# Optimization experiments

Measured on AMD Instinct MI355X. Metric: run time of the kernel, lower is better.

The kernel has to match this reference:

```python
import jax, jax.numpy as jnp
import numpy as np
from jax import lax

# Fixed dims from MSSMamba defaults
B_, L_, DM = 2, 8192, 256
NH, HP, NS = 4, 64, 8          # nheads, headdim, d_state
DIN = NH * HP                  # d_inner = 256
DPROJ = 2 * DIN + 2 * NS + NH  # 532


def setup_inputs() -> dict:
    key = jax.random.key(0)
    ks = jax.random.split(key, 16)
    f = lambda k, s, sc=1.0: jax.random.normal(k, s, jnp.float32) * sc
    inp = {
        'x_H': f(ks[0], (B_, L_, DM)),
        'x_V': f(ks[1], (B_, L_, DM)),
        'W_in_H': f(ks[2], (DM, 2 * DPROJ), 0.05),
        'W_in_V': f(ks[3], (DM, 2 * DPROJ), 0.05),
        'W_out_HF': f(ks[4], (DIN, DM), 0.05),
        'W_out_HB': f(ks[5], (DIN, DM), 0.05),
        'W_out_VF': f(ks[6], (DIN, DM), 0.05),
        'W_out_VB': f(ks[7], (DIN, DM), 0.05),
        'W_out': f(ks[8], (4 * DM, DM), 0.05),
    }
    for i, nm in enumerate(['HF', 'HB', 'VF', 'VB']):
        kd = jax.random.fold_in(ks[9], i)
        ka = jax.random.fold_in(ks[10], i)
        inp['dt_bias_' + nm] = f(kd, (NH,), 0.1)
        inp['A_log_' + nm] = jnp.log(jax.random.uniform(ka, (NH,), jnp.float32, 1.0, 16.0))
        inp['D_' + nm] = jnp.ones((NH,), jnp.float32)
    # per-batch permutation mapping vertical position -> horizontal position
    inp['v2h'] = jax.vmap(lambda k: jax.random.permutation(k, L_))(
        jax.random.split(ks[11], B_)).astype(jnp.int32)
    return inp


def _scan_dir(zxbcdt, dt_bias, A_log, D):
    # zxbcdt: [b, l, DPROJ] -> Mamba2-style selective scan, ngroups=1
    z = zxbcdt[..., :DIN].reshape(B_, L_, NH, HP)
    xBC = jax.nn.silu(zxbcdt[..., DIN:DIN + DIN + 2 * NS])
    x = xBC[..., :DIN].reshape(B_, L_, NH, HP)
    Bm = xBC[..., DIN:DIN + NS]      # [b, l, n]
    Cm = xBC[..., DIN + NS:]         # [b, l, n]
    dt = jax.nn.softplus(zxbcdt[..., -NH:] + dt_bias)  # [b, l, h]
    A = -jnp.exp(A_log)              # [h]
    dA = jnp.exp(dt * A)             # [b, l, h]
    dBx = jnp.einsum('blh,bln,blhp->blhpn', dt, Bm, x)  # [b,l,h,p,n]

    def step(state, inp):
        dA_t, dBx_t, C_t = inp
        state = dA_t[..., None, None] * state + dBx_t   # [b,h,p,n]
        y_t = jnp.einsum('bhpn,bn->bhp', state, C_t)
        return state, y_t

    init = jnp.zeros((B_, NH, HP, NS), dt.dtype)
    _, ys = lax.scan(step, init, (jnp.moveaxis(dA, 1, 0),
                                  jnp.moveaxis(dBx, 1, 0),
                                  jnp.moveaxis(Cm, 1, 0)))
    y = jnp.moveaxis(ys, 0, 1) + D[None, None, :, None] * x  # skip D*x
    y = y * jax.nn.silu(z)                                   # gate
    return y.reshape(B_, L_, DIN)


def reference(x_H, x_V, W_in_H, W_in_V,
              dt_bias_HF, dt_bias_HB, dt_bias_VF, dt_bias_VB,
              A_log_HF, A_log_HB, A_log_VF, A_log_VB,
              D_HF, D_HB, D_VF, D_VB,
              W_out_HF, W_out_HB, W_out_VF, W_out_VB,
              W_out, v2h):
    zx_HF, zx_HB = jnp.split(x_H @ W_in_H, 2, axis=-1)
    zx_VF, zx_VB = jnp.split(x_V @ W_in_V, 2, axis=-1)
    # note: source applies out_proj_HB to the HF branch (kept faithful)
    y_HF = _scan_dir(zx_HF, dt_bias_HF, A_log_HF, D_HF) @ W_out_HB
    y_HB = _scan_dir(zx_HB[:, ::-1], dt_bias_HB, A_log_HB, D_HB)[:, ::-1] @ W_out_HF
    y_VF = _scan_dir(zx_VF, dt_bias_VF, A_log_VF, D_VF) @ W_out_VB
    y_VB = _scan_dir(zx_VB[:, ::-1], dt_bias_VB, A_log_VB, D_VB)[:, ::-1] @ W_out_VF
    # remap vertical-ordered outputs to horizontal ordering (scatter by v2h)
    bidx = jnp.arange(B_)[:, None]
    y_VF = jnp.zeros_like(y_VF).at[bidx, v2h].set(y_VF)
    y_VB = jnp.zeros_like(y_VB).at[bidx, v2h].set(y_VB)
    cat = jnp.concatenate([y_HF, y_HB, y_VF, y_VB], axis=-1)  # [b, l, 4*d_model]
    return jax.nn.silu(cat) @ W_out
```

## Files before the change

### kernel.cpp

```cpp
#include <hip/hip_runtime.h>
#include <hip/hip_bf16.h>

#define B_N 2
#define L_N 8192
#define ROWS 16384
#define CHUNK 32
#define NCHUNK 256
#define GRP 16
#define NGRP 16
#define NPAD 1152

typedef __bf16 bf16x8 __attribute__((ext_vector_type(8)));
typedef float f32x4 __attribute__((ext_vector_type(4)));

__device__ __forceinline__ float siluf(float v) {
  return v * __builtin_amdgcn_rcpf(1.f + __expf(-v));
}
__device__ __forceinline__ float softplusf_(float v) {
  return fmaxf(v, 0.f) + log1pf(__expf(-fabsf(v)));
}
__device__ __forceinline__ unsigned short f2bf(float v) {
  union { __bf16 b; unsigned short u; } x;
  x.b = (__bf16)v;
  return x.u;
}
__device__ __forceinline__ float bf2f(unsigned short u) {
  union { unsigned u; float f; } x; x.u = ((unsigned)u) << 16;
  return x.f;
}

__device__ __forceinline__ void gload_lds16(const unsigned short* g, unsigned short* l) {
  __builtin_amdgcn_global_load_lds(
      (const __attribute__((address_space(1))) unsigned int*)g,
      (__attribute__((address_space(3))) unsigned int*)l, 16, 0, 0);
}

struct P4 { const float* p[4]; };
struct ScanConsts {
  const float* dt_bias[4];
  const float* A_log[4];
  const float* D[4];
};

__global__ __launch_bounds__(256) void k_prep(
    const float* __restrict__ xH, const float* __restrict__ xV,
    const float* __restrict__ WH, const float* __restrict__ WV,
    P4 ws, const float* __restrict__ W_out, const int* __restrict__ v2h, ScanConsts sc,
    unsigned short* __restrict__ xbf, float* __restrict__ dtv_arr, float* __restrict__ dA_arr,
    unsigned short* __restrict__ Wt_in, unsigned short* __restrict__ Wt_dirs,
    unsigned short* __restrict__ Wt_fin, int* __restrict__ inv) {
  __shared__ float xs[32][257];
  __shared__ float Wsm[8][260];
  int bid = blockIdx.x;
  int tid = threadIdx.x;
  if (bid < 1024) {
    const int mat = bid >> 9;
    const float* x = mat ? xV : xH;
    const float* W = mat ? WV : WH;
    const int r0 = (bid & 511) * 32;
    for (int i = tid; i < 2048; i += 256) {
      int c = i >> 8, k = i & 255;
      int sl = c >> 2, h = c & 3;
      Wsm[c][k] = W[(long)k * 1064 + sl * 532 + 528 + h];
    }
    for (int i = tid; i < 32 * 64; i += 256) {
      int rl = i >> 6, kq = (i & 63) * 4;
      float4 v = *(const float4*)(x + (long)(r0 + rl) * 256 + kq);
      xs[rl][kq + 0] = v.x; xs[rl][kq + 1] = v.y; xs[rl][kq + 2] = v.z; xs[rl][kq + 3] = v.w;
    }
    __syncthreads();
    for (int i = tid; i < 32 * 64; i += 256) {
      int rl = i >> 6, kq = (i & 63) * 4;
      ushort4 o;
      o.x = f2bf(xs[rl][kq + 0]);
      o.y = f2bf(xs[rl][kq + 1]);
      o.z = f2bf(xs[rl][kq + 2]);
      o.w = f2bf(xs[rl][kq + 3]);
      *(ushort4*)(xbf + (size_t)mat * ROWS * 256 + (long)(r0 + rl) * 256 + kq) = o;
    }
    const int rl = tid >> 3, c = tid & 7;
    float s = 0.f;
    #pragma unroll 8
    for (int k = 0; k < 256; ++k) s = fmaf(xs[rl][k], Wsm[c][k], s);
    const int sl = c >> 2, h = c & 3;
    const int dir = mat * 2 + sl;
    float dtv = softplusf_(s + sc.dt_bias[dir][h]);
    float dAv = __expf(dtv * (-__expf(sc.A_log[dir][h])));
    long o = ((long)dir * 4 + h) * ROWS + (r0 + rl);
    dtv_arr[o] = dtv;
    dA_arr[o] = dAv;
  } else if (bid < 3328) {
    int i = (bid - 1024) * 256 + tid;
    int z = i / (NPAD * 256);
    int rem = i - z * (NPAD * 256);
    int n = rem >> 8, k = rem & 255;
    const float* W = z ? WV : WH;
    int sl = n >= 544;
    int cc = n - (sl ? 544 : 0);
    float v = (cc < 532) ? W[(long)k * 1064 + sl * 532 + cc] : 0.f;
    Wt_in[i] = f2bf(v);
  } else if (bid < 4352) {
    int i = (bid - 3328) * 256 + tid;
    int d = i >> 16;
    int rem = i & 65535;
    int n = rem >> 8, k = rem & 255;
    Wt_dirs[i] = f2bf(ws.p[d][(long)k * 256 + n]);
  } else if (bid < 5376) {
    int i = (bid - 4352) * 256 + tid;
    int n = i >> 10, k = i & 1023;
    Wt_fin[i] = f2bf(W_out[(long)k * 256 + n]);
  } else {
    int m = (bid - 5376) * 256 + tid;
    if (m < ROWS) {
      int b = m >> 13;
      inv[b * L_N + v2h[m]] = m;
    }
  }
}

struct EpiIn {
  unsigned short* zraw;
  unsigned short* xraw;
  unsigned short* bc;
};

__global__ __launch_bounds__(256) void k_gemm_in(
    const unsigned short* __restrict__ Abase, const unsigned short* __restrict__ Btbase,
    EpiIn ep) {
  __shared__ unsigned short smem[24576];
  const int tid = threadIdx.x;
  const int lane = tid & 63;
  const int wid = tid >> 6;
  const int wm = wid & 1, wn = wid >> 1;
  const int q = lane >> 4, r = lane & 15;
  const int m0 = blockIdx.x * 128;
  const int n0 = blockIdx.y * 128;
  const int z = blockIdx.z;
  const unsigned short* A = Abase + (long)z * ROWS * 256;
  const unsigned short* Bt = Btbase + (long)z * NPAD * 256;

  int s_row[2], s_ch[2];
  #pragma unroll
  for (int i = 0; i < 2; ++i) {
    int idx = i * 256 + tid;
    s_row[i] = idx >> 2;
    s_ch[i] = (idx & 3) ^ ((s_row[i] >> 1) & 3);
  }

  auto stage = [&](int ti) {
    const int slot = ti % 3;
    const int kt = ti * 32;
    #pragma unroll
    for (int i = 0; i < 2; ++i) {
      gload_lds16(A + (long)(m0 + s_row[i]) * 256 + kt + s_ch[i] * 8,
                  smem + (size_t)slot * 4096 + (size_t)(i * 256 + wid * 64) * 8);
      gload_lds16(Bt + (long)(n0 + s_row[i]) * 256 + kt + s_ch[i] * 8,
                  smem + 12288 + (size_t)slot * 4096 + (size_t)(i * 256 + wid * 64) * 8);
    }
  };

  f32x4 acc[4][4] = {};
  const int swr = (r >> 1) & 3;

  stage(0);
  stage(1);

  #pragma unroll
  for (int i = 0; i < 8; ++i) {
    if (i < 7) asm volatile("s_waitcnt vmcnt(4)" ::: "memory");
    else       asm volatile("s_waitcnt vmcnt(0)" ::: "memory");
    __builtin_amdgcn_s_barrier();
    __builtin_amdgcn_sched_barrier(0);
    if (i + 2 < 8) stage(i + 2);
    const int slot = i % 3;
    bf16x8 af[4], bfr[4];
    #pragma unroll
    for (int mi = 0; mi < 4; ++mi)
      af[mi] = *(const bf16x8*)&smem[(size_t)slot * 4096 +
                                     ((wm * 64 + mi * 16 + r) * 4 + (q ^ swr)) * 8];
    #pragma unroll
    for (int ni = 0; ni < 4; ++ni)
      bfr[ni] = *(const bf16x8*)&smem[12288 + (size_t)slot * 4096 +
                                      ((wn * 64 + ni * 16 + r) * 4 + (q ^ swr)) * 8];
    __builtin_amdgcn_s_setprio(1);
    #pragma unroll
    for (int mi = 0; mi < 4; ++mi)
      #pragma unroll
      for (int ni = 0; ni < 4; ++ni)
        acc[mi][ni] = __builtin_amdgcn_mfma_f32_16x16x32_bf16(af[mi], bfr[ni], acc[mi][ni], 0, 0, 0);
    __builtin_amdgcn_s_setprio(0);
  }
  __syncthreads();

  unsigned short* tr = smem + wid * (16 * 72);
  #pragma unroll
  for (int mi = 0; mi < 4; ++mi) {
    #pragma unroll
    for (int ni = 0; ni < 4; ++ni)
      #pragma unroll
      for (int j = 0; j < 4; ++j)
        tr[(q * 4 + j) * 72 + ni * 16 + r] = f2bf(acc[mi][ni][j]);
    asm volatile("s_waitcnt lgkmcnt(0)" ::: "memory");
    #pragma unroll
    for (int pass = 0; pass < 2; ++pass) {
      int rl = pass * 8 + (lane >> 3);
      int c8 = (lane & 7) * 8;
      bf16x8 v = *(const bf16x8*)&tr[rl * 72 + c8];
      int row = m0 + wm * 64 + mi * 16 + rl;
      int col = n0 + wn * 64 + c8;
      int sl = col >= 544;
      int cc = col - (sl ? 544 : 0);
      if (cc < 528) {
        int dir = z * 2 + sl;
        if (cc < 256)
          *(bf16x8*)(ep.zraw + ((long)dir * ROWS + row) * 256 + cc) = v;
        else if (cc < 512)
          *(bf16x8*)(ep.xraw + ((long)dir * ROWS + row) * 256 + cc - 256) = v;
        else
          *(bf16x8*)(ep.bc + ((long)dir * ROWS + row) * 16 + cc - 512) = v;
      }
    }
    asm volatile("s_waitcnt lgkmcnt(0)" ::: "memory");
  }
}

__global__ __launch_bounds__(512) void k_fuse(
    const unsigned short* __restrict__ ybf,
    const unsigned short* __restrict__ Wt_dirs,
    const unsigned short* __restrict__ Wt_fin,
    const int* __restrict__ inv,
    float* __restrict__ out) {
  __shared__ unsigned short smf[47616];
  unsigned short* Ab = smf;
  unsigned short* Bb = smf + 6144;
  unsigned short* Tl = smf + 30720;
  float* Ttmp = (float*)(smf + 30720);
  const int tid = threadIdx.x;
  const int lane = tid & 63;
  const int wid = tid >> 6;
  const int wm = wid & 1, wn = wid >> 1;
  const int q = lane >> 4, r = lane & 15;
  const int r0 = blockIdx.x * 64;
  const int swr = (r >> 1) & 3;

  const int a_row = tid >> 2;
  const int a_ch = (tid & 3) ^ ((a_row >> 1) & 3);
  const long a_offH = (long)(r0 + a_row) * 256 + a_ch * 8;
  long a_offV = 0;
  if (tid < 256) a_offV = (long)inv[r0 + a_row] * 256 + a_ch * 8;
  int b_row[2], b_ch[2];
  #pragma unroll
  for (int rnd = 0; rnd < 2; ++rnd) {
    int idx = rnd * 512 + tid;
    b_row[rnd] = idx >> 2;
    b_ch[rnd] = (idx & 3) ^ ((b_row[rnd] >> 1) & 3);
  }

  auto stageT = [&](int g) {
    const int seg = g >> 3, ti = g & 7, kt = ti * 32;
    const int dl = seg >> 1;
    const int slot = g % 3;
    if ((seg & 1) == 0) {
      const long aoff = (dl >= 2) ? a_offV : a_offH;
      if (tid < 256)
        gload_lds16(ybf + (long)dl * ROWS * 256 + aoff + kt,
                    Ab + (size_t)slot * 2048 + (size_t)(wid * 64) * 8);
      #pragma unroll
      for (int rnd = 0; rnd < 2; ++rnd)
        gload_lds16(Wt_dirs + (long)dl * 65536 + (long)b_row[rnd] * 256 + kt + b_ch[rnd] * 8,
                    Bb + (size_t)slot * 8192 + (size_t)(rnd * 512 + wid * 64) * 8);
    } else {
      #pragma unroll
      for (int rnd = 0; rnd < 2; ++rnd)
        gload_lds16(Wt_fin + (long)b_row[rnd] * 1024 + dl * 256 + kt + b_ch[rnd] * 8,
                    Bb + (size_t)slot * 8192 + (size_t)(rnd * 512 + wid * 64) * 8);
    }
  };

  f32x4 acc_o[2][4] = {};

  stageT(0);
  stageT(1);

  #pragma unroll
  for (int d = 0; d < 4; ++d) {
    f32x4 acc_t[2][4] = {};
    #pragma unroll
    for (int i = 0; i < 8; ++i) {
      const int g = d * 16 + i;
      asm volatile("s_waitcnt vmcnt(2)" ::: "memory");
      __builtin_amdgcn_s_barrier();
      __builtin_amdgcn_sched_barrier(0);
      stageT(g + 2);
      const int slot = g % 3;
      bf16x8 af[2], bfr[4];
      #pragma unroll
      for (int mi = 0; mi < 2; ++mi)
        af[mi] = *(const bf16x8*)&Ab[(size_t)slot * 2048 +
                                     ((wm * 32 + mi * 16 + r) * 4 + (q ^ swr)) * 8];
      #pragma unroll
      for (int ni = 0; ni < 4; ++ni)
        bfr[ni] = *(const bf16x8*)&Bb[(size_t)slot * 8192 +
                                      ((wn * 64 + ni * 16 + r) * 4 + (q ^ swr)) * 8];
      __builtin_amdgcn_s_setprio(1);
      #pragma unroll
      for (int mi = 0; mi < 2; ++mi)
        #pragma unroll
        for (int ni = 0; ni < 4; ++ni)
          acc_t[mi][ni] = __builtin_amdgcn_mfma_f32_16x16x32_bf16(af[mi], bfr[ni], acc_t[mi][ni], 0, 0, 0);
      __builtin_amdgcn_s_setprio(0);
    }
    #pragma unroll
    for (int mi = 0; mi < 2; ++mi)
      #pragma unroll
      for (int ni = 0; ni < 4; ++ni)
        #pragma unroll
        for (int j = 0; j < 4; ++j)
          Tl[(wm * 32 + mi * 16 + q * 4 + j) * 264 + wn * 64 + ni * 16 + r] =
              f2bf(siluf(acc_t[mi][ni][j]));
    asm volatile("s_waitcnt lgkmcnt(0)" ::: "memory");
    #pragma unroll
    for (int i = 0; i < 8; ++i) {
      const int g = d * 16 + 8 + i;
      if (g < 63) asm volatile("s_waitcnt vmcnt(2)" ::: "memory");
      else        asm volatile("s_waitcnt vmcnt(0)" ::: "memory");
      __builtin_amdgcn_s_barrier();
      __builtin_amdgcn_sched_barrier(0);
      if (g + 2 < 64) stageT(g + 2);
      const int slot = g % 3;
      const int kt = i * 32;
      bf16x8 af[2], bfr[4];
      #pragma unroll
      for (int mi = 0; mi < 2; ++mi)
        af[mi] = *(const bf16x8*)&Tl[(wm * 32 + mi * 16 + r) * 264 + kt + q * 8];
      #pragma unroll
      for (int ni = 0; ni < 4; ++ni)
        bfr[ni] = *(const bf16x8*)&Bb[(size_t)slot * 8192 +
                                      ((wn * 64 + ni * 16 + r) * 4 + (q ^ swr)) * 8];
      __builtin_amdgcn_s_setprio(1);
      #pragma unroll
      for (int mi = 0; mi < 2; ++mi)
        #pragma unroll
        for (int ni = 0; ni < 4; ++ni)
          acc_o[mi][ni] = __builtin_amdgcn_mfma_f32_16x16x32_bf16(af[mi], bfr[ni], acc_o[mi][ni], 0, 0, 0);
      __builtin_amdgcn_s_setprio(0);
    }
  }

  __syncthreads();
  #pragma unroll
  for (int h = 0; h < 2; ++h) {
    if (wm == h) {
      #pragma unroll
      for (int mi = 0; mi < 2; ++mi)
        #pragma unroll
        for (int ni = 0; ni < 4; ++ni)
          #pragma unroll
          for (int j = 0; j < 4; ++j)
            Ttmp[(mi * 16 + q * 4 + j) * 260 + wn * 64 + ni * 16 + r] = acc_o[mi][ni][j];
    }
    __syncthreads();
    #pragma unroll
    for (int pass = 0; pass < 4; ++pass) {
      int id = pass * 512 + tid;
      int row = id >> 6, c4 = (id & 63) * 4;
      float4 v = *(const float4*)&Ttmp[row * 260 + c4];
      *(float4*)(out + (long)(r0 + h * 32 + row) * 256 + c4) = v;
    }
    if (h == 0) __syncthreads();
  }
}

struct ScanP {
  const unsigned short* xraw;
  const unsigned short* zraw;
  const unsigned short* bc;
  const float* dtv;
  const float* dA;
  const float* D[4];
};

__global__ __launch_bounds__(512) void k_scan1(ScanP sp, float* __restrict__ S,
                                               float* __restrict__ P) {
  __shared__ __align__(16) float Bst[8][CHUNK][8];
  __shared__ float dAs[8][CHUNK];
  const int tid = threadIdx.x;
  const int p = tid & 63;
  const int w = tid >> 6;
  const int c = blockIdx.x;
  const int d = blockIdx.y;
  const int bh = w;
  const int b = bh >> 2, h = bh & 3;
  const int rev = d & 1;
  const int t0 = c * CHUNK;
  if (p < CHUNK) {
    const int t = t0 + p;
    const int l = rev ? (L_N - 1 - t) : t;
    const int row = (b << 13) + l;
    uint4 bv = *(const uint4*)(sp.bc + ((long)d * ROWS + row) * 16);
    const unsigned short* bu = (const unsigned short*)&bv;
    float dtvv = sp.dtv[((long)d * 4 + h) * ROWS + row];
    dAs[w][p] = sp.dA[((long)d * 4 + h) * ROWS + row];
    #pragma unroll
    for (int n = 0; n < 8; ++n) Bst[w][p][n] = siluf(bf2f(bu[n])) * dtvv;
  }
  __syncthreads();

  float st[8] = {0, 0, 0, 0, 0, 0, 0, 0};
  float cumdA = 1.f;
  const int l0 = rev ? (L_N - 1 - t0) : t0;
  const unsigned short* xp = sp.xraw + ((long)d * ROWS + (b << 13) + l0) * 256 + h * 64 + p;
  const long stp = rev ? -256L : 256L;

  unsigned short xa[4], xb[4];
  #pragma unroll
  for (int j = 0; j < 4; ++j) xa[j] = xp[(long)j * stp];
  #pragma unroll
  for (int g = 0; g < 8; ++g) {
    if (g < 7) {
      #pragma unroll
      for (int j = 0; j < 4; ++j) xb[j] = xp[(long)((g + 1) * 4 + j) * stp];
    }
    #pragma unroll
    for (int j = 0; j < 4; ++j) {
      int s = g * 4 + j;
      float x = siluf(bf2f(xa[j]));
      float dA = dAs[w][s];
      f32x4 B0 = *(const f32x4*)&Bst[w][s][0];
      f32x4 B1 = *(const f32x4*)&Bst[w][s][4];
      cumdA *= dA;
      st[0] = fmaf(dA, st[0], x * B0[0]);
      st[1] = fmaf(dA, st[1], x * B0[1]);
      st[2] = fmaf(dA, st[2], x * B0[2]);
      st[3] = fmaf(dA, st[3], x * B0[3]);
      st[4] = fmaf(dA, st[4], x * B1[0]);
      st[5] = fmaf(dA, st[5], x * B1[1]);
      st[6] = fmaf(dA, st[6], x * B1[2]);
      st[7] = fmaf(dA, st[7], x * B1[3]);
    }
    #pragma unroll
    for (int j = 0; j < 4; ++j) xa[j] = xb[j];
  }
  float* Sp = S + ((((long)d * NCHUNK + c) * 8 + bh) * 64 + p) * 8;
  #pragma unroll
  for (int n = 0; n < 8; ++n) Sp[n] = st[n];
  if (p == 0) P[((long)d * NCHUNK + c) * 8 + bh] = cumdA;
}

__global__ __launch_bounds__(512) void k_scan2a(const float* __restrict__ S,
                                                const float* __restrict__ P,
                                                float* __restrict__ carry_loc,
                                                float* __restrict__ Sg,
                                                float* __restrict__ Pg) {
  __shared__ float Pl[GRP];
  const int tid = threadIdx.x;
  const int gid = blockIdx.x;
  const int g = gid & 15;
  const int dbh = gid >> 4;
  const int d = dbh >> 3, bh = dbh & 7;
  if (tid < GRP) Pl[tid] = P[((long)d * NCHUNK + g * GRP + tid) * 8 + bh];
  __syncthreads();
  float cy = 0.f;
  #pragma unroll
  for (int i = 0; i < GRP; ++i) {
    const int c = g * GRP + i;
    carry_loc[(((long)d * NCHUNK + c) * 8 + bh) * 512 + tid] = cy;
    const float Sv = S[(((long)d * NCHUNK + c) * 8 + bh) * 512 + tid];
    cy = fmaf(Pl[i], cy, Sv);
  }
  Sg[(((long)d * NGRP + g) * 8 + bh) * 512 + tid] = cy;
  if (tid == 0) {
    float pp = 1.f;
    #pragma unroll
    for (int i = 0; i < GRP; ++i) pp *= Pl[i];
    Pg[((long)d * NGRP + g) * 8 + bh] = pp;
  }
}

__global__ __launch_bounds__(512) void k_scan2b(const float* __restrict__ Sg,
                                                const float* __restrict__ Pg,
                                                float* __restrict__ gcarry) {
  __shared__ float Pgl[NGRP];
  const int tid = threadIdx.x;
  const int dbh = blockIdx.x;
  const int d = dbh >> 3, bh = dbh & 7;
  if (tid < NGRP) Pgl[tid] = Pg[((long)d * NGRP + tid) * 8 + bh];
  __syncthreads();
  float cy = 0.f;
  #pragma unroll
  for (int g = 0; g < NGRP; ++g) {
    gcarry[(((long)d * NGRP + g) * 8 + bh) * 512 + tid] = cy;
    const float Sv = Sg[(((long)d * NGRP + g) * 8 + bh) * 512 + tid];
    cy = fmaf(Pgl[g], cy, Sv);
  }
}

__global__ __launch_bounds__(512) void k_scan3(ScanP sp,
                                               const float* __restrict__ carry_loc,
                                               const float* __restrict__ gcarry,
                                               const float* __restrict__ Pc,
                                               unsigned short* __restrict__ ybf) {
  __shared__ __align__(16) float Bst[8][CHUNK][8];
  __shared__ __align__(16) float Cst[8][CHUNK][8];
  __shared__ float dAs[8][CHUNK];
  __shared__ float Pgr[8][GRP];
  const int tid = threadIdx.x;
  const int p = tid & 63;
  const int w = tid >> 6;
  const int c = blockIdx.x;
  const int d = blockIdx.y;
  const int bh = w;
  const int b = bh >> 2, h = bh & 3;
  const int rev = d & 1;
  const float Dv = sp.D[d][h];
  const int t0 = c * CHUNK;
  const int grp = c >> 4, ii = c & 15;
  if (p < ii) Pgr[w][p] = Pc[((long)d * NCHUNK + grp * GRP + p) * 8 + bh];
  if (p < CHUNK) {
    const int t = t0 + p;
    const int l = rev ? (L_N - 1 - t) : t;
    const int row = (b << 13) + l;
    const unsigned short* bp = sp.bc + ((long)d * ROWS + row) * 16;
    uint4 bv = *(const uint4*)bp;
    uint4 cv = *(const uint4*)(bp + 8);
    const unsigned short* bu = (const unsigned short*)&bv;
    const unsigned short* cu = (const unsigned short*)&cv;
    float dtvv = sp.dtv[((long)d * 4 + h) * ROWS + row];
    dAs[w][p] = sp.dA[((long)d * 4 + h) * ROWS + row];
    #pragma unroll
    for (int n = 0; n < 8; ++n) Bst[w][p][n] = siluf(bf2f(bu[n])) * dtvv;
    #pragma unroll
    for (int n = 0; n < 8; ++n) Cst[w][p][n] = siluf(bf2f(cu[n]));
  }
  __syncthreads();

  float pref = 1.f;
  for (int k = 0; k < ii; ++k) pref *= Pgr[w][k];
  float st[8];
  {
    const float* clp = carry_loc + ((((long)d * NCHUNK + c) * 8 + bh) * 64 + p) * 8;
    const float* gcp = gcarry + ((((long)d * NGRP + grp) * 8 + bh) * 64 + p) * 8;
    #pragma unroll
    for (int n = 0; n < 8; ++n) st[n] = fmaf(pref, gcp[n], clp[n]);
  }

  const int l0 = rev ? (L_N - 1 - t0) : t0;
  const long base = (long)(b << 13) + l0;
  const unsigned short* xp = sp.xraw + ((long)d * ROWS + base) * 256 + h * 64 + p;
  const unsigned short* zp = sp.zraw + ((long)d * ROWS + base) * 256 + h * 64 + p;
  unsigned short* yp = ybf + ((long)d * ROWS + base) * 256 + h * 64 + p;
  const long stp = rev ? -256L : 256L;

  unsigned short xa[4], xb[4], za[4], zb[4];
  #pragma unroll
  for (int j = 0; j < 4; ++j) { xa[j] = xp[(long)j * stp]; za[j] = zp[(long)j * stp]; }
  #pragma unroll
  for (int g = 0; g < 8; ++g) {
    if (g < 7) {
      #pragma unroll
      for (int j = 0; j < 4; ++j) {
        xb[j] = xp[(long)((g + 1) * 4 + j) * stp];
        zb[j] = zp[(long)((g + 1) * 4 + j) * stp];
      }
    }
    #pragma unroll
    for (int j = 0; j < 4; ++j) {
      int s = g * 4 + j;
      float x = siluf(bf2f(xa[j]));
      float zv = siluf(bf2f(za[j]));
      float dA = dAs[w][s];
      f32x4 B0 = *(const f32x4*)&Bst[w][s][0];
      f32x4 B1 = *(const f32x4*)&Bst[w][s][4];
      f32x4 C0 = *(const f32x4*)&Cst[w][s][0];
      f32x4 C1 = *(const f32x4*)&Cst[w][s][4];
      st[0] = fmaf(dA, st[0], x * B0[0]);
      st[1] = fmaf(dA, st[1], x * B0[1]);
      st[2] = fmaf(dA, st[2], x * B0[2]);
      st[3] = fmaf(dA, st[3], x * B0[3]);
      st[4] = fmaf(dA, st[4], x * B1[0]);
      st[5] = fmaf(dA, st[5], x * B1[1]);
      st[6] = fmaf(dA, st[6], x * B1[2]);
      st[7] = fmaf(dA, st[7], x * B1[3]);
      float y01 = fmaf(st[1], C0[1], st[0] * C0[0]);
      float y23 = fmaf(st[3], C0[3], st[2] * C0[2]);
      float y45 = fmaf(st[5], C1[1], st[4] * C1[0]);
      float y67 = fmaf(st[7], C1[3], st[6] * C1[2]);
      float y = (y01 + y23) + (y45 + y67);
      y = fmaf(Dv, x, y) * zv;
      yp[(long)s * stp] = f2bf(y);
    }
    #pragma unroll
    for (int j = 0; j < 4; ++j) { xa[j] = xb[j]; za[j] = zb[j]; }
  }
}

extern "C" void kernel_launch(void* const* d_in, const int* in_sizes, int n_in,
                              void* d_out, int out_size, void* d_ws, size_t ws_size,
                              hipStream_t stream) {
  const float* x_H = (const float*)d_in[0];
  const float* x_V = (const float*)d_in[1];
  const float* W_in_H = (const float*)d_in[2];
  const float* W_in_V = (const float*)d_in[3];
  const float* W_out_HF = (const float*)d_in[4];
  const float* W_out_HB = (const float*)d_in[5];
  const float* W_out_VF = (const float*)d_in[6];
  const float* W_out_VB = (const float*)d_in[7];
  const float* W_out = (const float*)d_in[8];
  const float* dt_bias_HF = (const float*)d_in[9];
  const float* A_log_HF = (const float*)d_in[10];
  const float* D_HF = (const float*)d_in[11];
  const float* dt_bias_HB = (const float*)d_in[12];
  const float* A_log_HB = (const float*)d_in[13];
  const float* D_HB = (const float*)d_in[14];
  const float* dt_bias_VF = (const float*)d_in[15];
  const float* A_log_VF = (const float*)d_in[16];
  const float* D_VF = (const float*)d_in[17];
  const float* dt_bias_VB = (const float*)d_in[18];
  const float* A_log_VB = (const float*)d_in[19];
  const float* D_VB = (const float*)d_in[20];
  const int* v2h = (const int*)d_in[21];

  char* ws = (char*)d_ws;
  size_t off = 0;
  auto alloc = [&](size_t bytes) {
    void* pp = ws + off;
    off = (off + bytes + 255) & ~(size_t)255;
    return pp;
  };
  unsigned short* xbf = (unsigned short*)alloc((size_t)2 * ROWS * 256 * 2);
  unsigned short* Wt_in = (unsigned short*)alloc((size_t)2 * NPAD * 256 * 2);
  unsigned short* Wt_dirs = (unsigned short*)alloc((size_t)4 * 65536 * 2);
  unsigned short* Wt_fin = (unsigned short*)alloc((size_t)256 * 1024 * 2);
  unsigned short* zraw = (unsigned short*)alloc((size_t)4 * ROWS * 256 * 2);
  unsigned short* xraw = (unsigned short*)alloc((size_t)4 * ROWS * 256 * 2);
  unsigned short* bc = (unsigned short*)alloc((size_t)4 * ROWS * 16 * 2);
  float* dtv_arr = (float*)alloc((size_t)16 * ROWS * 4);
  float* dA_arr = (float*)alloc((size_t)16 * ROWS * 4);
  unsigned short* ybf = (unsigned short*)alloc((size_t)4 * ROWS * 256 * 2);
  float* S = (float*)alloc((size_t)4 * NCHUNK * 8 * 512 * 4);
  float* P = (float*)alloc((size_t)4 * NCHUNK * 8 * 4);
  float* carry_loc = (float*)alloc((size_t)4 * NCHUNK * 8 * 512 * 4);
  float* Sg = (float*)alloc((size_t)4 * NGRP * 8 * 512 * 4);
  float* Pg = (float*)alloc((size_t)4 * NGRP * 8 * 4);
  float* gcarry = (float*)alloc((size_t)4 * NGRP * 8 * 512 * 4);
  int* inv = (int*)alloc((size_t)ROWS * 4);

  ScanConsts sc;
  sc.dt_bias[0] = dt_bias_HF; sc.dt_bias[1] = dt_bias_HB;
  sc.dt_bias[2] = dt_bias_VF; sc.dt_bias[3] = dt_bias_VB;
  sc.A_log[0] = A_log_HF; sc.A_log[1] = A_log_HB;
  sc.A_log[2] = A_log_VF; sc.A_log[3] = A_log_VB;
  sc.D[0] = D_HF; sc.D[1] = D_HB; sc.D[2] = D_VF; sc.D[3] = D_VB;

  P4 wdirs;
  wdirs.p[0] = W_out_HB; wdirs.p[1] = W_out_HF; wdirs.p[2] = W_out_VB; wdirs.p[3] = W_out_VF;

  k_prep<<<5440, 256, 0, stream>>>(x_H, x_V, W_in_H, W_in_V, wdirs, W_out, v2h, sc,
                                   xbf, dtv_arr, dA_arr, Wt_in, Wt_dirs, Wt_fin, inv);

  EpiIn ep; ep.zraw = zraw; ep.xraw = xraw; ep.bc = bc;

  k_gemm_in<<<dim3(ROWS / 128, NPAD / 128, 2), 256, 0, stream>>>(xbf, Wt_in, ep);

  ScanP sp;
  sp.xraw = xraw; sp.zraw = zraw; sp.bc = bc; sp.dtv = dtv_arr; sp.dA = dA_arr;
  sp.D[0] = D_HF; sp.D[1] = D_HB; sp.D[2] = D_VF; sp.D[3] = D_VB;

  k_scan1<<<dim3(NCHUNK, 4), 512, 0, stream>>>(sp, S, P);
  k_scan2a<<<512, 512, 0, stream>>>(S, P, carry_loc, Sg, Pg);
  k_scan2b<<<32, 512, 0, stream>>>(Sg, Pg, gcarry);
  k_scan3<<<dim3(NCHUNK, 4), 512, 0, stream>>>(sp, carry_loc, gcarry, P, ybf);

  k_fuse<<<256, 512, 0, stream>>>(ybf, Wt_dirs, Wt_fin, inv, (float*)d_out);

  (void)in_sizes; (void)n_in; (void)out_size; (void)ws_size;
}
```

Measured before the change: 241.6 us.

## Double scan chunk length and remap GEMM blocks for XCD locality

Scan chunks grow from 32 to 64 timesteps, which halves the number of chunks and groups and removes the p<CHUNK guard so all 64 lanes load per-step data. The input GEMM moves to a 1D grid whose block index is decoded so that consecutive M tiles land on the same XCD, aiming for better L2 reuse. Fewer chunks shorten the carry-propagation stages but make each serial chunk scan longer and reduce block-level parallelism. Some shared arrays in code not shown are sized by CHUNK, and scan3 still decodes chunk ids with hardcoded >>4 and &15, so correctness relies on those staying consistent with GRP.

```diff
diff --git a/kernel.cpp b/kernel.cpp
--- a/kernel.cpp
+++ b/kernel.cpp
@@ -4,10 +4,10 @@
 #define B_N 2
 #define L_N 8192
 #define ROWS 16384
-#define CHUNK 32
-#define NCHUNK 256
+#define CHUNK 64
+#define NCHUNK 128
 #define GRP 16
-#define NGRP 16
+#define NGRP 8
 #define NPAD 1152
 
 typedef __bf16 bf16x8 __attribute__((ext_vector_type(8)));
@@ -133,9 +133,12 @@
   const int wid = tid >> 6;
   const int wm = wid & 1, wn = wid >> 1;
   const int q = lane >> 4, r = lane & 15;
-  const int m0 = blockIdx.x * 128;
-  const int n0 = blockIdx.y * 128;
-  const int z = blockIdx.z;
+  const int hbid = blockIdx.x;
+  const int xcd = hbid & 7;
+  const int j = hbid >> 3;
+  const int m0 = (xcd * 16 + (j & 15)) * 128;
+  const int n0 = ((j >> 4) % 9) * 128;
+  const int z = j / 144;
   const unsigned short* A = Abase + (long)z * ROWS * 256;
   const unsigned short* Bt = Btbase + (long)z * NPAD * 256;
 
@@ -198,8 +201,8 @@
     #pragma unroll
     for (int ni = 0; ni < 4; ++ni)
       #pragma unroll
-      for (int j = 0; j < 4; ++j)
-        tr[(q * 4 + j) * 72 + ni * 16 + r] = f2bf(acc[mi][ni][j]);
+      for (int j2 = 0; j2 < 4; ++j2)
+        tr[(q * 4 + j2) * 72 + ni * 16 + r] = f2bf(acc[mi][ni][j2]);
     asm volatile("s_waitcnt lgkmcnt(0)" ::: "memory");
     #pragma unroll
     for (int pass = 0; pass < 2; ++pass) {
@@ -315,9 +318,9 @@
       #pragma unroll
       for (int ni = 0; ni < 4; ++ni)
         #pragma unroll
-        for (int j = 0; j < 4; ++j)
-          Tl[(wm * 32 + mi * 16 + q * 4 + j) * 264 + wn * 64 + ni * 16 + r] =
-              f2bf(siluf(acc_t[mi][ni][j]));
+        for (int jj = 0; jj < 4; ++jj)
+          Tl[(wm * 32 + mi * 16 + q * 4 + jj) * 264 + wn * 64 + ni * 16 + r] =
+              f2bf(siluf(acc_t[mi][ni][jj]));
     asm volatile("s_waitcnt lgkmcnt(0)" ::: "memory");
     #pragma unroll
     for (int i = 0; i < 8; ++i) {
@@ -356,8 +359,8 @@
         #pragma unroll
         for (int ni = 0; ni < 4; ++ni)
           #pragma unroll
-          for (int j = 0; j < 4; ++j)
-            Ttmp[(mi * 16 + q * 4 + j) * 260 + wn * 64 + ni * 16 + r] = acc_o[mi][ni][j];
+          for (int jj = 0; jj < 4; ++jj)
+            Ttmp[(mi * 16 + q * 4 + jj) * 260 + wn * 64 + ni * 16 + r] = acc_o[mi][ni][jj];
     }
     __syncthreads();
     #pragma unroll
@@ -393,7 +396,7 @@
   const int b = bh >> 2, h = bh & 3;
   const int rev = d & 1;
   const int t0 = c * CHUNK;
-  if (p < CHUNK) {
+  {
     const int t = t0 + p;
     const int l = rev ? (L_N - 1 - t) : t;
     const int row = (b << 13) + l;
@@ -416,8 +419,8 @@
   #pragma unroll
   for (int j = 0; j < 4; ++j) xa[j] = xp[(long)j * stp];
   #pragma unroll
-  for (int g = 0; g < 8; ++g) {
-    if (g < 7) {
+  for (int g = 0; g < CHUNK / 4; ++g) {
+    if (g < CHUNK / 4 - 1) {
       #pragma unroll
       for (int j = 0; j < 4; ++j) xb[j] = xp[(long)((g + 1) * 4 + j) * stp];
     }
@@ -455,8 +458,8 @@
   __shared__ float Pl[GRP];
   const int tid = threadIdx.x;
   const int gid = blockIdx.x;
-  const int g = gid & 15;
-  const int dbh = gid >> 4;
+  const int g = gid & (NGRP - 1);
+  const int dbh = gid >> 3;
   const int d = dbh >> 3, bh = dbh & 7;
   if (tid < GRP) Pl[tid] = P[((long)d * NCHUNK + g * GRP + tid) * 8 + bh];
   __syncthreads();
@@ -516,7 +519,7 @@
   const int t0 = c * CHUNK;
   const int grp = c >> 4, ii = c & 15;
   if (p < ii) Pgr[w][p] = Pc[((long)d * NCHUNK + grp * GRP + p) * 8 + bh];
-  if (p < CHUNK) {
+  {
     const int t = t0 + p;
     const int l = rev ? (L_N - 1 - t) : t;
     const int row = (b << 13) + l;
@@ -555,8 +558,8 @@
   #pragma unroll
   for (int j = 0; j < 4; ++j) { xa[j] = xp[(long)j * stp]; za[j] = zp[(long)j * stp]; }
   #pragma unroll
-  for (int g = 0; g < 8; ++g) {
-    if (g < 7) {
+  for (int g = 0; g < CHUNK / 4; ++g) {
+    if (g < CHUNK / 4 - 1) {
       #pragma unroll
       for (int j = 0; j < 4; ++j) {
         xb[j] = xp[(long)((g + 1) * 4 + j) * stp];
@@ -660,14 +663,14 @@
 
   EpiIn ep; ep.zraw = zraw; ep.xraw = xraw; ep.bc = bc;
 
-  k_gemm_in<<<dim3(ROWS / 128, NPAD / 128, 2), 256, 0, stream>>>(xbf, Wt_in, ep);
+  k_gemm_in<<<2304, 256, 0, stream>>>(xbf, Wt_in, ep);
 
   ScanP sp;
   sp.xraw = xraw; sp.zraw = zraw; sp.bc = bc; sp.dtv = dtv_arr; sp.dA = dA_arr;
   sp.D[0] = D_HF; sp.D[1] = D_HB; sp.D[2] = D_VF; sp.D[3] = D_VB;
 
   k_scan1<<<dim3(NCHUNK, 4), 512, 0, stream>>>(sp, S, P);
-  k_scan2a<<<512, 512, 0, stream>>>(S, P, carry_loc, Sg, Pg);
+  k_scan2a<<<32 * NGRP, 512, 0, stream>>>(S, P, carry_loc, Sg, Pg);
   k_scan2b<<<32, 512, 0, stream>>>(Sg, Pg, gcarry);
   k_scan3<<<dim3(NCHUNK, 4), 512, 0, stream>>>(sp, carry_loc, gcarry, P, ybf);
 
```

Result: no change. 237.0 us, median of 2 (-1.9%).
